# Kernel optimization log

Measured on AMD Instinct MI355X. Metric: run time of the kernel, lower is better.

The kernel has to match this reference:

```python
import jax, jax.numpy as jnp
import numpy as np

FORGET_BIAS = 1.0
PI_MIX = 0.25
SIGMA1 = float(np.exp(-1.0))
SIGMA2 = float(np.exp(-7.0))
LOG_2PI = float(np.log(2.0 * np.pi))


def _log_gauss(x, mu, sigma):
    return -0.5 * LOG_2PI - jnp.log(sigma) - 0.5 * ((x - mu) / sigma) ** 2


def _compute_kl(w, mu, sigma):
    # log q(w | mu, sigma) - log p(w) with scale-mixture Gaussian prior
    log_q = jnp.sum(_log_gauss(w, mu, sigma))
    lp1 = _log_gauss(w, 0.0, SIGMA1) + jnp.log(PI_MIX)
    lp2 = _log_gauss(w, 0.0, SIGMA2) + jnp.log(1.0 - PI_MIX)
    log_p = jnp.sum(jnp.logaddexp(lp1, lp2))
    return log_q - log_p


def _run_layer(x, h0, c0, weights, bias):
    # x: [S,B,H]; h0,c0: [B,H]; weights: [2H,4H]; bias: [4H]
    H = h0.shape[-1]

    def step(carry, x_t):
        h, c = carry
        gates = jnp.concatenate([x_t, h], axis=-1) @ weights + bias  # [B,4H]
        i, j, f, o = jnp.split(gates, 4, axis=-1)
        new_c = c * jax.nn.sigmoid(f + FORGET_BIAS) + jax.nn.sigmoid(i) * jnp.tanh(j)
        new_h = jnp.tanh(new_c) * jax.nn.sigmoid(o)
        return (new_h, new_c), new_h

    (h, c), out = jax.lax.scan(step, (h0, c0), x)
    return out, h, c


def setup_inputs() -> dict:
    key = jax.random.key(0)
    ks = jax.random.split(key, 5)
    S, B, H, L = 256, 64, 1024, 2
    x = jax.random.normal(ks[0], (S, B, H), dtype=jnp.float32)
    h0 = jax.random.normal(ks[1], (L, B, H), dtype=jnp.float32)
    c0 = jax.random.normal(ks[2], (L, B, H), dtype=jnp.float32)
    init_scale = 0.05
    mu = jax.random.uniform(ks[3], (L, 2 * H, 4 * H), jnp.float32, -init_scale, init_scale)
    rho = jax.random.uniform(ks[4], (L, 2 * H, 4 * H), jnp.float32, -4.0, -3.0)
    bias = jnp.zeros((L, 4 * H), dtype=jnp.float32)
    return {"x": x, "h0": h0, "c0": c0, "mu": mu, "rho": rho, "bias": bias}


def reference(x, h0, c0, mu, rho, bias):
    L = mu.shape[0]
    eps_key = jax.random.key(1)
    kl = jnp.float32(0.0)
    hs, cs = [], []
    out = None
    for l in range(L):
        sigma = jax.nn.softplus(rho[l]) + 1e-5
        eps = jax.random.normal(jax.random.fold_in(eps_key, l), mu[l].shape, dtype=mu.dtype)
        weights = mu[l] + eps * sigma
        # NOTE: original code feeds the SAME x into every layer (not the
        # previous layer's output) — replicated faithfully here.
        out, h, c = _run_layer(x, h0[l], c0[l], weights, bias[l])
        hs.append(h)
        cs.append(c)
        kl = kl + _compute_kl(weights, mu[l], sigma)
    h_stack = jnp.stack(hs, axis=0)
    c_stack = jnp.stack(cs, axis=0)
    return out, h_stack, c_stack, kl
```

## Files before the change

kernel.cpp:

```cpp
#include <hip/hip_runtime.h>
#include <cstdint>

#define WS_WT   0UL
#define WS_XBF  33554432UL
#define WS_HBUF 67108864UL
#define WS_KL   68157440UL
#define WS_ARR  68157504UL

typedef __attribute__((ext_vector_type(8))) short short8;
typedef __attribute__((ext_vector_type(4))) float f32x4;

__device__ __forceinline__ unsigned short f2bf(float f) {
  unsigned int u = __float_as_uint(f);
  u += 0x7FFFu + ((u >> 16) & 1u);
  return (unsigned short)(u >> 16);
}

__device__ __forceinline__ float sigm(float x) { return 1.0f / (1.0f + expf(-x)); }

__device__ __forceinline__ void tf_round(uint32_t& x0, uint32_t& x1, int r) {
  x0 += x1; x1 = (x1 << r) | (x1 >> (32 - r)); x1 ^= x0;
}
__device__ __forceinline__ void threefry2x32_dev(uint32_t k0, uint32_t k1,
                                                 uint32_t c0, uint32_t c1,
                                                 uint32_t& o0, uint32_t& o1) {
  uint32_t ks2 = k0 ^ k1 ^ 0x1BD11BDAu;
  uint32_t x0 = c0 + k0, x1 = c1 + k1;
  tf_round(x0,x1,13); tf_round(x0,x1,15); tf_round(x0,x1,26); tf_round(x0,x1,6);
  x0 += k1;  x1 += ks2 + 1u;
  tf_round(x0,x1,17); tf_round(x0,x1,29); tf_round(x0,x1,16); tf_round(x0,x1,24);
  x0 += ks2; x1 += k0 + 2u;
  tf_round(x0,x1,13); tf_round(x0,x1,15); tf_round(x0,x1,26); tf_round(x0,x1,6);
  x0 += k0;  x1 += k1 + 3u;
  tf_round(x0,x1,17); tf_round(x0,x1,29); tf_round(x0,x1,16); tf_round(x0,x1,24);
  x0 += k1;  x1 += ks2 + 4u;
  tf_round(x0,x1,13); tf_round(x0,x1,15); tf_round(x0,x1,26); tf_round(x0,x1,6);
  x0 += ks2; x1 += k0 + 5u;
  o0 = x0; o1 = x1;
}

__device__ __forceinline__ float erfinv_f32(float x) {
  float w = -log1pf(-x * x);
  float p;
  if (w < 5.0f) {
    w -= 2.5f;
    p = 2.81022636e-08f;
    p = fmaf(p, w, 3.43273939e-07f);
    p = fmaf(p, w, -3.5233877e-06f);
    p = fmaf(p, w, -4.39150654e-06f);
    p = fmaf(p, w, 0.00021858087f);
    p = fmaf(p, w, -0.00125372503f);
    p = fmaf(p, w, -0.00417768164f);
    p = fmaf(p, w, 0.246640727f);
    p = fmaf(p, w, 1.50140941f);
  } else {
    w = sqrtf(w) - 3.0f;
    p = -0.000200214257f;
    p = fmaf(p, w, 0.000100950558f);
    p = fmaf(p, w, 0.00134934322f);
    p = fmaf(p, w, -0.00367342844f);
    p = fmaf(p, w, 0.00573950773f);
    p = fmaf(p, w, -0.0076224613f);
    p = fmaf(p, w, 0.00943887047f);
    p = fmaf(p, w, 1.00167406f);
    p = fmaf(p, w, 2.83297682f);
  }
  return p * x;
}

__device__ __forceinline__ float bits_to_normal(uint32_t b) {
  float f = __uint_as_float((b >> 9) | 0x3f800000u) - 1.0f;
  float u = fmaf(f, 2.0f, -0.99999994f);
  u = fmaxf(-0.99999994f, u);
  return 1.41421356f * erfinv_f32(u);
}

__device__ __forceinline__ double kl_elem(float w, float eps, float sigma) {
  float logq = -0.91893853320f - logf(sigma) - 0.5f * eps * eps;
  float t1 = w * 2.71828182846f;
  float lp1 = -1.3052328943f - 0.5f * t1 * t1;
  float t2 = w * 1096.6331584f;
  float lp2 = 5.7933793944f - 0.5f * t2 * t2;
  float mx = fmaxf(lp1, lp2);
  float logp = mx + log1pf(expf(fminf(lp1, lp2) - mx));
  return (double)logq - (double)logp;
}

__global__ __launch_bounds__(256) void gen_weights(
    const float* __restrict__ mu, const float* __restrict__ rho,
    unsigned short* __restrict__ Wt, double* __restrict__ klsum,
    uint32_t ka0, uint32_t ka1, uint32_t kb0, uint32_t kb1)
{
  const int bid = blockIdx.x;
  const int l = bid >> 12;
  const int rem = bid & 4095;
  const int cb = rem >> 6, kb = rem & 63;
  const int tid = threadIdx.x;
  const int cc = tid >> 2, kg = tid & 3;
  const int col = cb * 64 + cc;
  const uint32_t K0 = l ? kb0 : ka0, K1 = l ? kb1 : ka1;
  const float* muL  = mu  + (size_t)l * 8388608;
  const float* rhoL = rho + (size_t)l * 8388608;
  const int kbase = kb * 16 + kg * 4;

  double kl = 0.0;
  unsigned short wlo[4], whi[4];
#pragma unroll
  for (int u = 0; u < 4; ++u) {
    const int kp = kbase + u;
    const uint32_t i = (uint32_t)(kp * 4096 + col);
    uint32_t r0, r1;
    threefry2x32_dev(K0, K1, i, i + 4194304u, r0, r1);
    {
      const float e = bits_to_normal(r0);
      const size_t off = (size_t)kp * 4096 + col;
      const float sg = log1pf(expf(rhoL[off])) + 1e-5f;
      const float w = fmaf(e, sg, muL[off]);
      kl += kl_elem(w, e, sg);
      wlo[u] = f2bf(w);
    }
    {
      const float e = bits_to_normal(r1);
      const size_t off = (size_t)(kp + 1024) * 4096 + col;
      const float sg = log1pf(expf(rhoL[off])) + 1e-5f;
      const float w = fmaf(e, sg, muL[off]);
      kl += kl_elem(w, e, sg);
      whi[u] = f2bf(w);
    }
  }
  const size_t wbase = ((size_t)(l * 4096 + col)) * 2048 + kbase;
  *(ushort4*)(Wt + wbase)        = make_ushort4(wlo[0], wlo[1], wlo[2], wlo[3]);
  *(ushort4*)(Wt + wbase + 1024) = make_ushort4(whi[0], whi[1], whi[2], whi[3]);

#pragma unroll
  for (int off = 32; off > 0; off >>= 1) kl += __shfl_down(kl, off, 64);
  __shared__ double part[4];
  const int lane = tid & 63, wv = tid >> 6;
  if (lane == 0) part[wv] = kl;
  __syncthreads();
  if (tid == 0) atomicAdd(klsum, part[0] + part[1] + part[2] + part[3]);
}

__global__ __launch_bounds__(256) void cvt_inputs(
    const float* __restrict__ x, const float* __restrict__ h0,
    unsigned short* __restrict__ xbf, unsigned short* __restrict__ hbuf)
{
  const int total = 4227072;
  for (int idx = blockIdx.x * 256 + threadIdx.x; idx < total; idx += gridDim.x * 256) {
    if (idx < 4194304) {
      float4 v = ((const float4*)x)[idx];
      ((ushort4*)xbf)[idx] = make_ushort4(f2bf(v.x), f2bf(v.y), f2bf(v.z), f2bf(v.w));
    } else {
      const int j = idx - 4194304;
      float4 v = ((const float4*)h0)[j];
      ((ushort4*)hbuf)[j] = make_ushort4(f2bf(v.x), f2bf(v.y), f2bf(v.z), f2bf(v.w));
    }
  }
}

__global__ __launch_bounds__(256) void lstm_rec(
    const unsigned short* __restrict__ Wt, const unsigned short* __restrict__ xbf,
    unsigned short* __restrict__ hbuf, const float* __restrict__ c0,
    const float* __restrict__ bias, float* __restrict__ outp,
    int* __restrict__ arrive)
{
  extern __shared__ char lds[];
  const int tid = threadIdx.x;
  const int lane = tid & 63;
  const int wv = tid >> 6;
  const int blk = blockIdx.x;
  const int layer = blk >> 7;
  const int bi = blk & 127;
  const int hc0 = bi << 3;

  {
    const int g = wv;
    const int c = lane >> 3;
    const int q = lane & 7;
    const int cw = g * 8 + c;
    const unsigned short* src = Wt + (size_t)(layer * 4096 + g * 1024 + hc0 + c) * 2048;
    const int swz = (cw & 7) << 4;
    for (int it = 0; it < 32; ++it) {
      const int k = it * 64 + q * 8;
      short8 v = *(const short8*)(src + k);
      const int byte = (cw << 12) + k * 2;
      *(short8*)(lds + (byte ^ swz)) = v;
    }
  }
  __syncthreads();

  const int g4 = lane >> 4;
  const int c16 = lane & 15;
  const int myrow = wv * 16 + c16;
  const int klane = g4 * 8;
  const int cw0 = c16, cw1 = 16 + c16;
  const int bb0 = (cw0 << 12) + klane * 2, sz0 = (cw0 & 7) << 4;
  const int bb1 = (cw1 << 12) + klane * 2, sz1 = (cw1 & 7) << 4;

  const int hc = lane & 7;
  const bool act = (lane & 8) == 0;
  float cst[4];
  {
    const size_t base = (size_t)layer * 65536 + (size_t)(wv * 16 + g4 * 4) * 1024 + hc0 + hc;
#pragma unroll
    for (int r = 0; r < 4; ++r) cst[r] = act ? c0[base + r * 1024] : 0.0f;
  }
  float bi_i = 0, bi_j = 0, bi_f = 0, bi_o = 0;
  if (act) {
    bi_i = bias[layer * 4096 + hc0 + hc];
    bi_j = bias[layer * 4096 + 1024 + hc0 + hc];
    bi_f = bias[layer * 4096 + 2048 + hc0 + hc];
    bi_o = bias[layer * 4096 + 3072 + hc0 + hc];
  }
  int* arr = arrive + layer * 257;

  for (int t = 0; t < 256; ++t) {
    f32x4 a0 = {0.f, 0.f, 0.f, 0.f}, a1 = {0.f, 0.f, 0.f, 0.f};
    const unsigned short* xa = xbf + (size_t)(t * 64 + myrow) * 1024 + klane;
#pragma unroll 4
    for (int kk = 0; kk < 32; ++kk) {
      short8 av = *(const short8*)(xa + kk * 32);
      short8 b0 = *(const short8*)(lds + ((bb0 + kk * 64) ^ sz0));
      short8 b1 = *(const short8*)(lds + ((bb1 + kk * 64) ^ sz1));
      a0 = __builtin_amdgcn_mfma_f32_16x16x32_bf16(av, b0, a0, 0, 0, 0);
      a1 = __builtin_amdgcn_mfma_f32_16x16x32_bf16(av, b1, a1, 0, 0, 0);
    }
    if (t > 0) {
      if (tid == 0) {
        while (__hip_atomic_load(arr + t, __ATOMIC_RELAXED, __HIP_MEMORY_SCOPE_AGENT) < 128)
          __builtin_amdgcn_s_sleep(1);
        __builtin_amdgcn_fence(__ATOMIC_ACQUIRE, "agent");
      }
      __syncthreads();
    }
    const unsigned short* ha = hbuf + (size_t)(((t & 3) * 2 + layer) * 64 + myrow) * 1024 + klane;
#pragma unroll 4
    for (int kk = 0; kk < 32; ++kk) {
      short8 av = *(const short8*)(ha + kk * 32);
      const int kb2 = (32 + kk) * 64;
      short8 b0 = *(const short8*)(lds + ((bb0 + kb2) ^ sz0));
      short8 b1 = *(const short8*)(lds + ((bb1 + kb2) ^ sz1));
      a0 = __builtin_amdgcn_mfma_f32_16x16x32_bf16(av, b0, a0, 0, 0, 0);
      a1 = __builtin_amdgcn_mfma_f32_16x16x32_bf16(av, b1, a1, 0, 0, 0);
    }
    float pj[4], po[4];
#pragma unroll
    for (int r = 0; r < 4; ++r) {
      pj[r] = __shfl_xor(a0[r], 8, 64);
      po[r] = __shfl_xor(a1[r], 8, 64);
    }
    if (act) {
      const int slotw = (t + 1) & 3;
      unsigned short* hw = hbuf + (size_t)((slotw * 2 + layer) * 64) * 1024;
      float* op = outp + (size_t)t * 65536;
#pragma unroll
      for (int r = 0; r < 4; ++r) {
        const float iv = a0[r] + bi_i, jv = pj[r] + bi_j;
        const float fv = a1[r] + bi_f, ov = po[r] + bi_o;
        const float nc = cst[r] * sigm(fv + 1.0f) + sigm(iv) * tanhf(jv);
        const float nh = tanhf(nc) * sigm(ov);
        cst[r] = nc;
        const int b = wv * 16 + g4 * 4 + r;
        hw[(size_t)b * 1024 + hc0 + hc] = f2bf(nh);
        if (layer == 1) op[(size_t)b * 1024 + hc0 + hc] = nh;
        if (t == 255) {
          outp[16777216 + (size_t)layer * 65536 + (size_t)b * 1024 + hc0 + hc] = nh;
          outp[16908288 + (size_t)layer * 65536 + (size_t)b * 1024 + hc0 + hc] = nc;
        }
      }
    }
    __syncthreads();
    if (tid == 0)
      __hip_atomic_fetch_add(arr + t + 1, 1, __ATOMIC_RELEASE, __HIP_MEMORY_SCOPE_AGENT);
  }
}

__global__ void finalize_kl(const double* __restrict__ klsum, float* __restrict__ outp) {
  outp[17039360] = (float)(*klsum);
}

static void host_threefry(uint32_t k0, uint32_t k1, uint32_t c0, uint32_t c1,
                          uint32_t& o0, uint32_t& o1) {
  auto rot = [](uint32_t x, int r) { return (x << r) | (x >> (32 - r)); };
  const int ra[4] = {13, 15, 26, 6}, rb[4] = {17, 29, 16, 24};
  uint32_t ks2 = k0 ^ k1 ^ 0x1BD11BDAu, x0 = c0 + k0, x1 = c1 + k1;
  for (int i = 0; i < 4; ++i) { x0 += x1; x1 = rot(x1, ra[i]); x1 ^= x0; } x0 += k1;  x1 += ks2 + 1u;
  for (int i = 0; i < 4; ++i) { x0 += x1; x1 = rot(x1, rb[i]); x1 ^= x0; } x0 += ks2; x1 += k0 + 2u;
  for (int i = 0; i < 4; ++i) { x0 += x1; x1 = rot(x1, ra[i]); x1 ^= x0; } x0 += k0;  x1 += k1 + 3u;
  for (int i = 0; i < 4; ++i) { x0 += x1; x1 = rot(x1, rb[i]); x1 ^= x0; } x0 += k1;  x1 += ks2 + 4u;
  for (int i = 0; i < 4; ++i) { x0 += x1; x1 = rot(x1, ra[i]); x1 ^= x0; } x0 += ks2; x1 += k0 + 5u;
  o0 = x0; o1 = x1;
}

extern "C" void kernel_launch(void* const* d_in, const int* in_sizes, int n_in,
                              void* d_out, int out_size, void* d_ws, size_t ws_size,
                              hipStream_t stream) {
  const float* x    = (const float*)d_in[0];
  const float* h0   = (const float*)d_in[1];
  const float* c0   = (const float*)d_in[2];
  const float* mu   = (const float*)d_in[3];
  const float* rho  = (const float*)d_in[4];
  const float* bias = (const float*)d_in[5];
  float* outp = (float*)d_out;
  char* ws = (char*)d_ws;

  unsigned short* Wt   = (unsigned short*)(ws + WS_WT);
  unsigned short* xbf  = (unsigned short*)(ws + WS_XBF);
  unsigned short* hbuf = (unsigned short*)(ws + WS_HBUF);
  double* klsum        = (double*)(ws + WS_KL);
  int* arrive          = (int*)(ws + WS_ARR);

  hipMemsetAsync(ws + WS_KL, 0, 4096, stream);

  uint32_t ka0, ka1, kb0, kb1;
  host_threefry(0u, 1u, 0u, 0u, ka0, ka1);
  host_threefry(0u, 1u, 0u, 1u, kb0, kb1);

  gen_weights<<<8192, 256, 0, stream>>>(mu, rho, Wt, klsum, ka0, ka1, kb0, kb1);
  cvt_inputs<<<8192, 256, 0, stream>>>(x, h0, xbf, hbuf);

  hipFuncSetAttribute((const void*)lstm_rec,
                      hipFuncAttributeMaxDynamicSharedMemorySize, 131072);
  lstm_rec<<<256, 256, 131072, stream>>>(Wt, xbf, hbuf, c0, bias, outp, arrive);
  finalize_kl<<<1, 1, 0, stream>>>(klsum, outp);
}
```

Baseline: 4.080 ms.

## Keep weights in registers, stage h in LDS, widen blocks to 512 threads

The recurrent kernel now holds each lane's weight fragment (64 short8) in VGPRs instead of LDS, and uses 512 threads split into row and column wave groups. Each block cooperatively loads h_{t-1} from global into swizzled LDS with agent-scope atomic loads, so only one copy is read per block rather than per wave. Every thread now spins on the arrival counter instead of one thread plus a block barrier, and gate results are gathered through an LDS scratch so each thread applies the LSTM cell to one element. This aims to cut LDS weight traffic and redundant global h reads on the per-step critical path. The cost is very high register pressure (possible spills or low occupancy) and extra barriers.

```diff
diff --git a/kernel.cpp b/kernel.cpp
--- a/kernel.cpp
+++ b/kernel.cpp
@@ -9,6 +9,7 @@
 
 typedef __attribute__((ext_vector_type(8))) short short8;
 typedef __attribute__((ext_vector_type(4))) float f32x4;
+typedef __attribute__((ext_vector_type(2))) unsigned long long ull2;
 
 __device__ __forceinline__ unsigned short f2bf(float f) {
   unsigned int u = __float_as_uint(f);
@@ -158,13 +159,16 @@
   }
 }
 
-__global__ __launch_bounds__(256) void lstm_rec(
+__global__ __launch_bounds__(512) void lstm_rec(
     const unsigned short* __restrict__ Wt, const unsigned short* __restrict__ xbf,
     unsigned short* __restrict__ hbuf, const float* __restrict__ c0,
     const float* __restrict__ bias, float* __restrict__ outp,
     int* __restrict__ arrive)
 {
   extern __shared__ char lds[];
+  char* hst = lds;
+  float* gb = (float*)(lds + 131072);
+
   const int tid = threadIdx.x;
   const int lane = tid & 63;
   const int wv = tid >> 6;
@@ -173,104 +177,103 @@
   const int bi = blk & 127;
   const int hc0 = bi << 3;
 
+  const int rowg = wv & 3, colg = wv >> 2;
+  const int lc = colg * 16 + (lane & 15);
+  const int g = lc >> 3, hcl_b = lc & 7;
+  const int kof = (lane >> 4) * 8;
+  const int row = rowg * 16 + (lane & 15);
+
+  short8 B[64];
   {
-    const int g = wv;
-    const int c = lane >> 3;
-    const int q = lane & 7;
-    const int cw = g * 8 + c;
-    const unsigned short* src = Wt + (size_t)(layer * 4096 + g * 1024 + hc0 + c) * 2048;
-    const int swz = (cw & 7) << 4;
-    for (int it = 0; it < 32; ++it) {
-      const int k = it * 64 + q * 8;
-      short8 v = *(const short8*)(src + k);
-      const int byte = (cw << 12) + k * 2;
-      *(short8*)(lds + (byte ^ swz)) = v;
-    }
-  }
-  __syncthreads();
-
-  const int g4 = lane >> 4;
-  const int c16 = lane & 15;
-  const int myrow = wv * 16 + c16;
-  const int klane = g4 * 8;
-  const int cw0 = c16, cw1 = 16 + c16;
-  const int bb0 = (cw0 << 12) + klane * 2, sz0 = (cw0 & 7) << 4;
-  const int bb1 = (cw1 << 12) + klane * 2, sz1 = (cw1 & 7) << 4;
-
-  const int hc = lane & 7;
-  const bool act = (lane & 8) == 0;
-  float cst[4];
-  {
-    const size_t base = (size_t)layer * 65536 + (size_t)(wv * 16 + g4 * 4) * 1024 + hc0 + hc;
-#pragma unroll
-    for (int r = 0; r < 4; ++r) cst[r] = act ? c0[base + r * 1024] : 0.0f;
-  }
-  float bi_i = 0, bi_j = 0, bi_f = 0, bi_o = 0;
-  if (act) {
-    bi_i = bias[layer * 4096 + hc0 + hc];
-    bi_j = bias[layer * 4096 + 1024 + hc0 + hc];
-    bi_f = bias[layer * 4096 + 2048 + hc0 + hc];
-    bi_o = bias[layer * 4096 + 3072 + hc0 + hc];
-  }
+    const unsigned short* wrow =
+        Wt + ((size_t)(layer * 4096 + g * 1024 + hc0 + hcl_b)) * 2048 + kof;
+#pragma unroll
+    for (int kc = 0; kc < 64; ++kc) B[kc] = *(const short8*)(wrow + kc * 32);
+  }
+
+  const int er = tid >> 3, ehc = tid & 7;
+  float creg = c0[(size_t)layer * 65536 + (size_t)er * 1024 + hc0 + ehc];
+  const float b_i = bias[layer * 4096 + hc0 + ehc];
+  const float b_j = bias[layer * 4096 + 1024 + hc0 + ehc];
+  const float b_f = bias[layer * 4096 + 2048 + hc0 + ehc];
+  const float b_o = bias[layer * 4096 + 3072 + hc0 + ehc];
+
+  const int sr = wv * 8 + ((lane >> 3) & 7);
+  const int ks8 = lane & 7;
   int* arr = arrive + layer * 257;
 
+  const int hrd_base = row * 2048 + kof * 2;
+  const int hrd_swz = (row & 7) << 4;
+  const int swr_swz = (sr & 7) << 4;
+
   for (int t = 0; t < 256; ++t) {
-    f32x4 a0 = {0.f, 0.f, 0.f, 0.f}, a1 = {0.f, 0.f, 0.f, 0.f};
-    const unsigned short* xa = xbf + (size_t)(t * 64 + myrow) * 1024 + klane;
-#pragma unroll 4
-    for (int kk = 0; kk < 32; ++kk) {
-      short8 av = *(const short8*)(xa + kk * 32);
-      short8 b0 = *(const short8*)(lds + ((bb0 + kk * 64) ^ sz0));
-      short8 b1 = *(const short8*)(lds + ((bb1 + kk * 64) ^ sz1));
-      a0 = __builtin_amdgcn_mfma_f32_16x16x32_bf16(av, b0, a0, 0, 0, 0);
-      a1 = __builtin_amdgcn_mfma_f32_16x16x32_bf16(av, b1, a1, 0, 0, 0);
-    }
+    f32x4 acc = {0.f, 0.f, 0.f, 0.f};
+    {
+      const unsigned short* xa = xbf + ((size_t)t * 64 + row) * 1024 + kof;
+#pragma unroll
+      for (int kc = 0; kc < 32; ++kc)
+        acc = __builtin_amdgcn_mfma_f32_16x16x32_bf16(
+            *(const short8*)(xa + kc * 32), B[kc], acc, 0, 0, 0);
+    }
+
     if (t > 0) {
-      if (tid == 0) {
-        while (__hip_atomic_load(arr + t, __ATOMIC_RELAXED, __HIP_MEMORY_SCOPE_AGENT) < 128)
-          __builtin_amdgcn_s_sleep(1);
-        __builtin_amdgcn_fence(__ATOMIC_ACQUIRE, "agent");
+      while (__hip_atomic_load(arr + t, __ATOMIC_RELAXED, __HIP_MEMORY_SCOPE_AGENT) < 128)
+        __builtin_amdgcn_s_sleep(2);
+      __builtin_amdgcn_sched_barrier(0);
+    }
+
+    {
+      const unsigned long long* hs = (const unsigned long long*)
+          (hbuf + ((size_t)((t & 3) * 2 + layer) * 64 + sr) * 1024);
+      unsigned long long v[32];
+#pragma unroll
+      for (int i = 0; i < 16; ++i) {
+        const int e8 = ks8 * 2 + i * 16;
+        v[2 * i]     = __hip_atomic_load(hs + e8,     __ATOMIC_RELAXED, __HIP_MEMORY_SCOPE_AGENT);
+        v[2 * i + 1] = __hip_atomic_load(hs + e8 + 1, __ATOMIC_RELAXED, __HIP_MEMORY_SCOPE_AGENT);
       }
-      __syncthreads();
-    }
-    const unsigned short* ha = hbuf + (size_t)(((t & 3) * 2 + layer) * 64 + myrow) * 1024 + klane;
-#pragma unroll 4
-    for (int kk = 0; kk < 32; ++kk) {
-      short8 av = *(const short8*)(ha + kk * 32);
-      const int kb2 = (32 + kk) * 64;
-      short8 b0 = *(const short8*)(lds + ((bb0 + kb2) ^ sz0));
-      short8 b1 = *(const short8*)(lds + ((bb1 + kb2) ^ sz1));
-      a0 = __builtin_amdgcn_mfma_f32_16x16x32_bf16(av, b0, a0, 0, 0, 0);
-      a1 = __builtin_amdgcn_mfma_f32_16x16x32_bf16(av, b1, a1, 0, 0, 0);
-    }
-    float pj[4], po[4];
-#pragma unroll
-    for (int r = 0; r < 4; ++r) {
-      pj[r] = __shfl_xor(a0[r], 8, 64);
-      po[r] = __shfl_xor(a1[r], 8, 64);
-    }
-    if (act) {
-      const int slotw = (t + 1) & 3;
-      unsigned short* hw = hbuf + (size_t)((slotw * 2 + layer) * 64) * 1024;
-      float* op = outp + (size_t)t * 65536;
-#pragma unroll
-      for (int r = 0; r < 4; ++r) {
-        const float iv = a0[r] + bi_i, jv = pj[r] + bi_j;
-        const float fv = a1[r] + bi_f, ov = po[r] + bi_o;
-        const float nc = cst[r] * sigm(fv + 1.0f) + sigm(iv) * tanhf(jv);
-        const float nh = tanhf(nc) * sigm(ov);
-        cst[r] = nc;
-        const int b = wv * 16 + g4 * 4 + r;
-        hw[(size_t)b * 1024 + hc0 + hc] = f2bf(nh);
-        if (layer == 1) op[(size_t)b * 1024 + hc0 + hc] = nh;
-        if (t == 255) {
-          outp[16777216 + (size_t)layer * 65536 + (size_t)b * 1024 + hc0 + hc] = nh;
-          outp[16908288 + (size_t)layer * 65536 + (size_t)b * 1024 + hc0 + hc] = nc;
-        }
+#pragma unroll
+      for (int i = 0; i < 16; ++i) {
+        const int k = ks8 * 8 + i * 64;
+        const int byte = (sr * 2048 + 2 * k) ^ swr_swz;
+        ull2 vv; vv.x = v[2 * i]; vv.y = v[2 * i + 1];
+        *(ull2*)(hst + byte) = vv;
       }
     }
     __syncthreads();
-    if (tid == 0)
+
+#pragma unroll
+    for (int kc = 0; kc < 32; ++kc) {
+      short8 av = *(const short8*)(hst + ((hrd_base + kc * 64) ^ hrd_swz));
+      acc = __builtin_amdgcn_mfma_f32_16x16x32_bf16(av, B[32 + kc], acc, 0, 0, 0);
+    }
+
+    {
+      const int rbase = rowg * 16 + (lane >> 4) * 4;
+#pragma unroll
+      for (int q = 0; q < 4; ++q) gb[(rbase + q) * 33 + lc] = acc[q];
+    }
+    __syncthreads();
+
+    {
+      const float i_ = gb[er * 33 + ehc] + b_i;
+      const float j_ = gb[er * 33 + 8 + ehc] + b_j;
+      const float f_ = gb[er * 33 + 16 + ehc] + b_f;
+      const float o_ = gb[er * 33 + 24 + ehc] + b_o;
+      const float nc = creg * sigm(f_ + 1.0f) + sigm(i_) * tanhf(j_);
+      const float nh = tanhf(nc) * sigm(o_);
+      creg = nc;
+      unsigned short* hw = hbuf + ((size_t)(((t + 1) & 3) * 2 + layer) * 64 + er) * 1024;
+      hw[hc0 + ehc] = f2bf(nh);
+      if (layer == 1) outp[(size_t)t * 65536 + (size_t)er * 1024 + hc0 + ehc] = nh;
+      if (t == 255) {
+        outp[16777216 + (size_t)layer * 65536 + (size_t)er * 1024 + hc0 + ehc] = nh;
+        outp[16908288 + (size_t)layer * 65536 + (size_t)er * 1024 + hc0 + ehc] = nc;
+      }
+    }
+    __syncthreads();
+
+    if (tid == 0 && t < 255)
       __hip_atomic_fetch_add(arr + t + 1, 1, __ATOMIC_RELEASE, __HIP_MEMORY_SCOPE_AGENT);
   }
 }
@@ -319,8 +322,9 @@
   gen_weights<<<8192, 256, 0, stream>>>(mu, rho, Wt, klsum, ka0, ka1, kb0, kb1);
   cvt_inputs<<<8192, 256, 0, stream>>>(x, h0, xbf, hbuf);
 
+  const int lds_bytes = 131072 + 64 * 33 * 4;
   hipFuncSetAttribute((const void*)lstm_rec,
-                      hipFuncAttributeMaxDynamicSharedMemorySize, 131072);
-  lstm_rec<<<256, 256, 131072, stream>>>(Wt, xbf, hbuf, c0, bias, outp, arrive);
+                      hipFuncAttributeMaxDynamicSharedMemorySize, lds_bytes);
+  lstm_rec<<<256, 512, lds_bytes, stream>>>(Wt, xbf, hbuf, c0, bias, outp, arrive);
   finalize_kl<<<1, 1, 0, stream>>>(klsum, outp);
 }
```

Measured after the change: 9.497 ms. 2.33x slower.
